# Kernel tuning notes

Hardware: AMD Instinct MI355X
Metric: run time of the kernel (lower is better)

The kernel has to match this reference:

```python
import jax, jax.numpy as jnp
import numpy as np

N_NODES = 50000
N_EDGES = 800000
IN_C = 128
HID_C = 2 * IN_C  # 256
OUT_C = 128
NEG_SLOPE = 0.2


def _gat_layer(x, edge_src, edge_dst, W, a_src, a_dst, b, n_nodes):
    # x: [N, Fin], W: [Fin, Fout], a_src/a_dst: [Fout], b: [Fout]
    h = x @ W                                   # [N, Fout]
    alpha_src = h @ a_src                       # [N]
    alpha_dst = h @ a_dst                       # [N]
    e = alpha_src[edge_src] + alpha_dst[edge_dst]           # [E]
    e = jnp.where(e > 0, e, NEG_SLOPE * e)      # LeakyReLU(0.2)
    # segment softmax over incoming edges of each destination node
    m = jax.ops.segment_max(e, edge_dst, num_segments=n_nodes)  # [N]
    w = jnp.exp(e - m[edge_dst])                               # [E]
    z = jax.ops.segment_sum(w, edge_dst, num_segments=n_nodes)  # [N]
    alpha = w / z[edge_dst]                                     # [E]
    # scatter-aggregate messages
    out = jax.ops.segment_sum(alpha[:, None] * h[edge_src], edge_dst,
                              num_segments=n_nodes)             # [N, Fout]
    return out + b


def setup_inputs() -> dict:
    key = jax.random.key(0)
    ks = jax.random.split(key, 12)
    x = jax.random.normal(ks[0], (N_NODES, IN_C), dtype=jnp.float32)
    edge_index = jax.random.randint(ks[1], (2, N_EDGES), 0, N_NODES, dtype=jnp.int32)
    def glorot(k, shape):
        fan_in = shape[0] if len(shape) == 2 else shape[0]
        return jax.random.normal(k, shape, dtype=jnp.float32) / np.sqrt(fan_in)
    W1 = glorot(ks[2], (IN_C, HID_C))
    a1_src = glorot(ks[3], (HID_C,))
    a1_dst = glorot(ks[4], (HID_C,))
    b1 = jnp.zeros((HID_C,), dtype=jnp.float32)
    W2 = glorot(ks[5], (HID_C, OUT_C))
    a2_src = glorot(ks[6], (OUT_C,))
    a2_dst = glorot(ks[7], (OUT_C,))
    b2 = jnp.zeros((OUT_C,), dtype=jnp.float32)
    return {"x": x, "edge_index": edge_index, "W1": W1, "a1_src": a1_src,
            "a1_dst": a1_dst, "b1": b1, "W2": W2, "a2_src": a2_src,
            "a2_dst": a2_dst, "b2": b2}


def reference(x, edge_index, W1, a1_src, a1_dst, b1, W2, a2_src, a2_dst, b2):
    n = x.shape[0]
    # PyG GATConv default: add self-loops
    loops = jnp.arange(n, dtype=edge_index.dtype)
    src = jnp.concatenate([edge_index[0], loops])
    dst = jnp.concatenate([edge_index[1], loops])
    h = _gat_layer(x, src, dst, W1, a1_src, a1_dst, b1, n)
    h = jax.nn.relu(h)
    out = _gat_layer(h, src, dst, W2, a2_src, a2_dst, b2, n)
    return out
```

## Files before the change

kernel.cpp:

```cpp
#include <hip/hip_runtime.h>
#include <hip/hip_bf16.h>
#include <math.h>

#define N_NODES 50000
#define N_EDGESX 800000
#define E_TOT   (N_EDGESX + N_NODES)
#define IN_C 128
#define HID_C 256
#define OUT_C 128
#define NEG_SLOPE 0.2f

typedef __attribute__((ext_vector_type(8))) short short8;
typedef __attribute__((ext_vector_type(4))) float floatx4;
typedef __attribute__((ext_vector_type(2))) float floatx2;

__device__ __forceinline__ float bf2f(short s) {
    unsigned u = ((unsigned)(unsigned short)s) << 16;
    float f; __builtin_memcpy(&f, &u, 4); return f;
}
__device__ __forceinline__ short f2bf(float f) {
    unsigned u; __builtin_memcpy(&u, &f, 4);
    unsigned r = (u + 0x7FFFu + ((u >> 16) & 1u)) >> 16;
    return (short)r;
}

template<int KROWS, int NCOLS>
__global__ __launch_bounds__(256)
void gemv_p_kernel(const float* __restrict__ W, const float* __restrict__ a_s,
                   const float* __restrict__ a_d, float* __restrict__ ps, float* __restrict__ pd) {
    int t = threadIdx.x;
    int k = t & (KROWS - 1);
    const float* av = (t < KROWS) ? a_s : a_d;
    float* pv = (t < KROWS) ? ps : pd;
    const float* row = W + (size_t)k * NCOLS;
    float s = 0.f;
    for (int n = 0; n < NCOLS; ++n) s += row[n] * av[n];
    pv[k] = s;
}

__global__ __launch_bounds__(256)
void alpha_x_kernel(const float* __restrict__ x, const float* __restrict__ ps,
                    const float* __restrict__ pd, float* __restrict__ as_out,
                    float* __restrict__ ad_out, short* __restrict__ xb) {
    int gt = blockIdx.x * blockDim.x + threadIdx.x;
    int node = gt >> 6, lane = gt & 63;
    if (node >= N_NODES) return;
    floatx2 xv = *(const floatx2*)&x[(size_t)node * IN_C + lane * 2];
    floatx2 s2 = *(const floatx2*)&ps[lane * 2];
    floatx2 d2 = *(const floatx2*)&pd[lane * 2];
    float s = xv[0] * s2[0] + xv[1] * s2[1];
    float d = xv[0] * d2[0] + xv[1] * d2[1];
    unsigned pack = (unsigned)(unsigned short)f2bf(xv[0]) | ((unsigned)(unsigned short)f2bf(xv[1]) << 16);
    *(unsigned*)&xb[(size_t)node * IN_C + lane * 2] = pack;
    #pragma unroll
    for (int off = 32; off; off >>= 1) {
        s += __shfl_down(s, off);
        d += __shfl_down(d, off);
    }
    if (lane == 0) { as_out[node] = s; ad_out[node] = d; }
}

__global__ void count_kernel(const int* __restrict__ dst, int* __restrict__ cnt) {
    int i = blockIdx.x * blockDim.x + threadIdx.x;
    if (i < E_TOT) {
        int d = (i < N_EDGESX) ? dst[i] : (i - N_EDGESX);
        atomicAdd(&cnt[d], 1);
    }
}

#define NBLK ((N_NODES + 1023) / 1024)

__global__ __launch_bounds__(1024)
void scan_a_kernel(const int* __restrict__ cnt, int* __restrict__ row_ptr, int* __restrict__ bsum) {
    __shared__ int buf[1024];
    int tid = threadIdx.x;
    int idx = blockIdx.x * 1024 + tid;
    int v = (idx < N_NODES) ? cnt[idx] : 0;
    buf[tid] = v;
    __syncthreads();
    for (int off = 1; off < 1024; off <<= 1) {
        int t = (tid >= off) ? buf[tid - off] : 0;
        __syncthreads();
        buf[tid] += t;
        __syncthreads();
    }
    if (idx < N_NODES) row_ptr[idx] = buf[tid] - v;
    if (tid == 1023) bsum[blockIdx.x] = buf[1023];
}

__global__ void scan_b_kernel(int* __restrict__ bsum, int* __restrict__ row_ptr) {
    int lane = threadIdx.x;
    int v = (lane < NBLK) ? bsum[lane] : 0;
    int s = v;
    #pragma unroll
    for (int off = 1; off < 64; off <<= 1) {
        int t = __shfl_up(s, off);
        if (lane >= off) s += t;
    }
    if (lane < NBLK) bsum[lane] = s - v;
    if (lane == 63) row_ptr[N_NODES] = s;
}

__global__ __launch_bounds__(1024)
void scan_c_kernel(int* __restrict__ row_ptr, const int* __restrict__ bsum, int* __restrict__ cursor) {
    int idx = blockIdx.x * 1024 + threadIdx.x;
    if (idx < N_NODES) {
        int v = row_ptr[idx] + bsum[blockIdx.x];
        row_ptr[idx] = v;
        cursor[idx] = v;
    }
}

__global__ void scatter_kernel(const int* __restrict__ src, const int* __restrict__ dst,
                               int* __restrict__ cursor, int* __restrict__ esrc) {
    int i = blockIdx.x * blockDim.x + threadIdx.x;
    if (i < E_TOT) {
        int s, d;
        if (i < N_EDGESX) { s = src[i]; d = dst[i]; }
        else { s = i - N_EDGESX; d = s; }
        int pos = atomicAdd(&cursor[d], 1);
        esrc[pos] = s;
    }
}

__global__ __launch_bounds__(256)
void fill_edst_kernel(const int* __restrict__ row_ptr, int* __restrict__ edst) {
    int gt = blockIdx.x * blockDim.x + threadIdx.x;
    int node = gt >> 6, lane = gt & 63;
    if (node >= N_NODES) return;
    int beg = row_ptr[node], end = row_ptr[node + 1];
    for (int i = beg + lane; i < end; i += 64) edst[i] = node;
}

__global__ void ew_kernel(const int* __restrict__ esrc, const int* __restrict__ edst,
                          const float* __restrict__ as_in, const float* __restrict__ ad_in,
                          float* __restrict__ ew) {
    int i = blockIdx.x * blockDim.x + threadIdx.x;
    if (i >= E_TOT) return;
    float e = as_in[esrc[i]] + ad_in[edst[i]];
    ew[i] = e > 0.f ? e : NEG_SLOPE * e;
}

__global__ void splitT_kernel(const float* __restrict__ W, short* __restrict__ th,
                              short* __restrict__ tl, int K, int N) {
    int i = blockIdx.x * blockDim.x + threadIdx.x;
    if (i >= K * N) return;
    int k = i / N, n = i - k * N;
    float f = W[i];
    short hb = f2bf(f);
    th[n * K + k] = hb;
    tl[n * K + k] = f2bf(f - bf2f(hb));
}

template<int K, int OUTMODE>
__global__ __launch_bounds__(256)
void gemm_mfma(const short* __restrict__ Ah, const short* __restrict__ Al,
               const short* __restrict__ Bth, const short* __restrict__ Btl,
               int N, const float* __restrict__ bias,
               short* __restrict__ C0, short* __restrict__ C1) {
    __shared__ short Ah_s[128][40];
    __shared__ short Al_s[128][40];
    __shared__ short Bh_s[64][40];
    __shared__ short Bl_s[64][40];
    int tid = threadIdx.x;
    int lane = tid & 63, wave = tid >> 6;
    int wr = wave >> 1, wc = wave & 1;
    int bm = blockIdx.y * 128, bn = blockIdx.x * 64;
    int l15 = lane & 15, kf = (lane >> 4) * 8;

    floatx4 acc[4][2];
    #pragma unroll
    for (int i = 0; i < 4; ++i)
        #pragma unroll
        for (int j = 0; j < 2; ++j) acc[i][j] = (floatx4){0.f, 0.f, 0.f, 0.f};

    int arow = tid >> 1, ac0 = (tid & 1) * 16;
    int brow = tid >> 2, bc0 = (tid & 3) * 8;
    int agm = bm + arow;
    bool aval = agm < N_NODES;

    for (int k0 = 0; k0 < K; k0 += 32) {
        short8 va0 = {0,0,0,0,0,0,0,0}, va1 = va0, vl0 = va0, vl1 = va0;
        if (aval) {
            const short* pa = Ah + (size_t)agm * K + k0 + ac0;
            va0 = *(const short8*)pa; va1 = *(const short8*)(pa + 8);
            const short* pl = Al + (size_t)agm * K + k0 + ac0;
            vl0 = *(const short8*)pl; vl1 = *(const short8*)(pl + 8);
        }
        *(short8*)&Ah_s[arow][ac0]     = va0;
        *(short8*)&Ah_s[arow][ac0 + 8] = va1;
        *(short8*)&Al_s[arow][ac0]     = vl0;
        *(short8*)&Al_s[arow][ac0 + 8] = vl1;
        {
            const short* pb = Bth + (size_t)(bn + brow) * K + k0 + bc0;
            *(short8*)&Bh_s[brow][bc0] = *(const short8*)pb;
            const short* pb2 = Btl + (size_t)(bn + brow) * K + k0 + bc0;
            *(short8*)&Bl_s[brow][bc0] = *(const short8*)pb2;
        }
        __syncthreads();
        short8 afh[4], afl[4], bfh[2], bfl[2];
        #pragma unroll
        for (int mr = 0; mr < 4; ++mr) {
            int r = wr * 64 + mr * 16 + l15;
            afh[mr] = *(const short8*)&Ah_s[r][kf];
            afl[mr] = *(const short8*)&Al_s[r][kf];
        }
        #pragma unroll
        for (int nr = 0; nr < 2; ++nr) {
            int c = wc * 32 + nr * 16 + l15;
            bfh[nr] = *(const short8*)&Bh_s[c][kf];
            bfl[nr] = *(const short8*)&Bl_s[c][kf];
        }
        #pragma unroll
        for (int mr = 0; mr < 4; ++mr)
            #pragma unroll
            for (int nr = 0; nr < 2; ++nr) {
                acc[mr][nr] = __builtin_amdgcn_mfma_f32_16x16x32_bf16(afh[mr], bfh[nr], acc[mr][nr], 0, 0, 0);
                acc[mr][nr] = __builtin_amdgcn_mfma_f32_16x16x32_bf16(afh[mr], bfl[nr], acc[mr][nr], 0, 0, 0);
                acc[mr][nr] = __builtin_amdgcn_mfma_f32_16x16x32_bf16(afl[mr], bfh[nr], acc[mr][nr], 0, 0, 0);
            }
        __syncthreads();
    }
    float bv[2];
    if (OUTMODE == 2) {
        #pragma unroll
        for (int nr = 0; nr < 2; ++nr) bv[nr] = bias[bn + wc * 32 + nr * 16 + l15];
    }
    #pragma unroll
    for (int mr = 0; mr < 4; ++mr) {
        #pragma unroll
        for (int reg = 0; reg < 4; ++reg) {
            int gr = bm + wr * 64 + mr * 16 + (lane >> 4) * 4 + reg;
            if (gr < N_NODES) {
                #pragma unroll
                for (int nr = 0; nr < 2; ++nr) {
                    int gc = bn + wc * 32 + nr * 16 + l15;
                    float v = acc[mr][nr][reg];
                    if (OUTMODE == 1) {
                        C0[(size_t)gr * N + gc] = f2bf(v);
                    } else {
                        v = fmaxf(v + bv[nr], 0.f);
                        short hb = f2bf(v);
                        C0[(size_t)gr * N + gc] = hb;
                        C1[(size_t)gr * N + gc] = f2bf(v - bf2f(hb));
                    }
                }
            }
        }
    }
}

__global__ __launch_bounds__(256)
void alpha_bf16_128(const short* __restrict__ h, const float* __restrict__ a_src,
                    const float* __restrict__ a_dst, float* __restrict__ as_out,
                    float* __restrict__ ad_out) {
    int gt = blockIdx.x * blockDim.x + threadIdx.x;
    int node = gt >> 6, lane = gt & 63;
    if (node >= N_NODES) return;
    unsigned u = *(const unsigned*)&h[(size_t)node * OUT_C + lane * 2];
    float v0 = bf2f((short)(u & 0xFFFFu));
    float v1 = bf2f((short)(u >> 16));
    floatx2 as2 = *(const floatx2*)&a_src[lane * 2];
    floatx2 ad2 = *(const floatx2*)&a_dst[lane * 2];
    float s = v0 * as2[0] + v1 * as2[1];
    float d = v0 * ad2[0] + v1 * ad2[1];
    #pragma unroll
    for (int off = 32; off; off >>= 1) {
        s += __shfl_down(s, off);
        d += __shfl_down(d, off);
    }
    if (lane == 0) { as_out[node] = s; ad_out[node] = d; }
}

template<int OUT>
__global__ __launch_bounds__(256)
void aggregate_kernel(const short* __restrict__ h, const float* __restrict__ ew,
                      const int* __restrict__ row_ptr, const int* __restrict__ esrc,
                      const float* __restrict__ bias,
                      short* __restrict__ o_hi, short* __restrict__ o_lo,
                      float* __restrict__ o_f32) {
    int gt = blockIdx.x * blockDim.x + threadIdx.x;
    int node = gt >> 6, lane = gt & 63;
    if (node >= N_NODES) return;
    int beg = row_ptr[node], end = row_ptr[node + 1];

    float ml = -1e30f, zl = 0.f;
    for (int i = beg + lane; i < end; i += 64) {
        float e = ew[i];
        float mn = fmaxf(ml, e);
        zl = zl * __expf(ml - mn) + __expf(e - mn);
        ml = mn;
    }
    #pragma unroll
    for (int off = 32; off; off >>= 1) {
        float mo = __shfl_xor(ml, off);
        float zo = __shfl_xor(zl, off);
        float mn = fmaxf(ml, mo);
        zl = zl * __expf(ml - mn) + zo * __expf(mo - mn);
        ml = mn;
    }
    float m = ml;
    float inv_z = 1.f / zl;

    int grp = lane >> 4, l = lane & 15;
    float acc[8] = {};
    int i = beg;
    for (; i + 4 < end; i += 8) {
        int e0 = i + grp;
        int e1 = i + 4 + grp;
        bool v1 = e1 < end;
        int s0 = esrc[e0];
        int s1 = esrc[v1 ? e1 : beg];
        float w0 = __expf(ew[e0] - m) * inv_z;
        float w1 = v1 ? __expf(ew[e1] - m) * inv_z : 0.f;
        short8 hv0 = *(const short8*)&h[(size_t)s0 * 128 + l * 8];
        short8 hv1 = *(const short8*)&h[(size_t)s1 * 128 + l * 8];
        #pragma unroll
        for (int j = 0; j < 8; ++j) acc[j] += w0 * bf2f(hv0[j]);
        #pragma unroll
        for (int j = 0; j < 8; ++j) acc[j] += w1 * bf2f(hv1[j]);
    }
    if (i < end) {
        int e = i + grp;
        bool v = e < end;
        int s = esrc[v ? e : beg];
        float w = v ? __expf(ew[e] - m) * inv_z : 0.f;
        short8 hv = *(const short8*)&h[(size_t)s * 128 + l * 8];
        #pragma unroll
        for (int j = 0; j < 8; ++j) acc[j] += w * bf2f(hv[j]);
    }
    #pragma unroll
    for (int j = 0; j < 8; ++j) {
        acc[j] += __shfl_xor(acc[j], 16);
        acc[j] += __shfl_xor(acc[j], 32);
    }

    if (lane < 16) {
        if (OUT == 0) {
            short8 oh, ol;
            #pragma unroll
            for (int j = 0; j < 8; ++j) {
                short hb = f2bf(acc[j]);
                oh[j] = hb;
                ol[j] = f2bf(acc[j] - bf2f(hb));
            }
            *(short8*)&o_hi[(size_t)node * 128 + l * 8] = oh;
            *(short8*)&o_lo[(size_t)node * 128 + l * 8] = ol;
        } else {
            const float* brow = &bias[l * 8];
            floatx4 o0, o1;
            #pragma unroll
            for (int j = 0; j < 4; ++j) {
                o0[j] = acc[j] + brow[j];
                o1[j] = acc[j + 4] + brow[j + 4];
            }
            float* orow = &o_f32[(size_t)node * 128 + l * 8];
            *(floatx4*)orow = o0;
            *(floatx4*)(orow + 4) = o1;
        }
    }
}

extern "C" void kernel_launch(void* const* d_in, const int* in_sizes, int n_in,
                              void* d_out, int out_size, void* d_ws, size_t ws_size,
                              hipStream_t stream) {
    const float* x   = (const float*)d_in[0];
    const int*   ei  = (const int*)d_in[1];
    const float* W1  = (const float*)d_in[2];
    const float* a1s = (const float*)d_in[3];
    const float* a1d = (const float*)d_in[4];
    const float* b1  = (const float*)d_in[5];
    const float* W2  = (const float*)d_in[6];
    const float* a2s = (const float*)d_in[7];
    const float* a2d = (const float*)d_in[8];
    const float* b2  = (const float*)d_in[9];
    float* out = (float*)d_out;

    const int* e_src = ei;
    const int* e_dst = ei + N_EDGESX;

    char* ws = (char*)d_ws;
    const size_t OFF_XB   = 0;
    const size_t OFF_UH   = 12800000;
    const size_t OFF_UL   = 25600000;
    const size_t OFF_G1H  = 38400000;
    const size_t OFF_G1L  = 64000000;
    const size_t OFF_H2   = 89600000;
    const size_t OFF_W1TH = 102400000;
    const size_t OFF_W1TL = 102465536;
    const size_t OFF_W2TH = 102531072;
    const size_t OFF_W2TL = 102596608;
    const size_t OFF_P1S  = 102662144;
    const size_t OFF_P1D  = 102662656;
    const size_t OFF_AS   = 102663168;
    const size_t OFF_AD   = 102863360;
    const size_t OFF_RP   = 103063552;
    const size_t OFF_CNT  = 103264000;
    const size_t OFF_CUR  = 103464192;
    const size_t OFF_BSUM = 103664384;
    const size_t OFF_ESRC = 103664640;
    const size_t OFF_EDST = 107064640;
    const size_t OFF_EW   = 110464640;

    short* xb   = (short*)(ws + OFF_XB);
    short* uh   = (short*)(ws + OFF_UH);
    short* ul   = (short*)(ws + OFF_UL);
    short* g1h  = (short*)(ws + OFF_G1H);
    short* g1l  = (short*)(ws + OFF_G1L);
    short* h2   = (short*)(ws + OFF_H2);
    short* w1th = (short*)(ws + OFF_W1TH);
    short* w1tl = (short*)(ws + OFF_W1TL);
    short* w2th = (short*)(ws + OFF_W2TH);
    short* w2tl = (short*)(ws + OFF_W2TL);
    float* p1s  = (float*)(ws + OFF_P1S);
    float* p1d  = (float*)(ws + OFF_P1D);
    float* as_b = (float*)(ws + OFF_AS);
    float* ad_b = (float*)(ws + OFF_AD);
    int* row_ptr = (int*)(ws + OFF_RP);
    int* cnt     = (int*)(ws + OFF_CNT);
    int* cursor  = (int*)(ws + OFF_CUR);
    int* bsum    = (int*)(ws + OFF_BSUM);
    int* esrc    = (int*)(ws + OFF_ESRC);
    int* edst    = (int*)(ws + OFF_EDST);
    float* ewb   = (float*)(ws + OFF_EW);

    int egrid = (E_TOT + 255) / 256;
    int ngrid = (N_NODES * 64 + 255) / 256;

    gemv_p_kernel<IN_C, HID_C><<<1, 256, 0, stream>>>(W1, a1s, a1d, p1s, p1d);
    alpha_x_kernel<<<ngrid, 256, 0, stream>>>(x, p1s, p1d, as_b, ad_b, xb);

    hipMemsetAsync(cnt, 0, N_NODES * sizeof(int), stream);
    count_kernel<<<egrid, 256, 0, stream>>>(e_dst, cnt);
    scan_a_kernel<<<NBLK, 1024, 0, stream>>>(cnt, row_ptr, bsum);
    scan_b_kernel<<<1, 64, 0, stream>>>(bsum, row_ptr);
    scan_c_kernel<<<NBLK, 1024, 0, stream>>>(row_ptr, bsum, cursor);
    scatter_kernel<<<egrid, 256, 0, stream>>>(e_src, e_dst, cursor, esrc);
    fill_edst_kernel<<<ngrid, 256, 0, stream>>>(row_ptr, edst);
    ew_kernel<<<egrid, 256, 0, stream>>>(esrc, edst, as_b, ad_b, ewb);

    splitT_kernel<<<(IN_C * HID_C + 255) / 256, 256, 0, stream>>>(W1, w1th, w1tl, IN_C, HID_C);
    splitT_kernel<<<(HID_C * OUT_C + 255) / 256, 256, 0, stream>>>(W2, w2th, w2tl, HID_C, OUT_C);

    aggregate_kernel<0><<<ngrid, 256, 0, stream>>>(xb, ewb, row_ptr, esrc, nullptr, uh, ul, nullptr);
    gemm_mfma<IN_C, 2><<<dim3(HID_C / 64, (N_NODES + 127) / 128), 256, 0, stream>>>(
        uh, ul, w1th, w1tl, HID_C, b1, g1h, g1l);

    gemm_mfma<HID_C, 1><<<dim3(OUT_C / 64, (N_NODES + 127) / 128), 256, 0, stream>>>(
        g1h, g1l, w2th, w2tl, OUT_C, nullptr, h2, nullptr);
    alpha_bf16_128<<<ngrid, 256, 0, stream>>>(h2, a2s, a2d, as_b, ad_b);
    ew_kernel<<<egrid, 256, 0, stream>>>(esrc, edst, as_b, ad_b, ewb);
    aggregate_kernel<1><<<ngrid, 256, 0, stream>>>(h2, ewb, row_ptr, esrc, b2, nullptr, nullptr, out);
}
```

Before: 365.2 us.

## Build CSR via two-pass bucketed binning with shared-memory atomics, fuse edge weights

Replaces the global-atomic count and scatter CSR build with a two-level bucketing scheme. Edges are first binned into 100-node buckets using per-block shared histograms and a staging buffer. Per-bucket kernels then count and scatter with shared-memory atomics. The first-layer edge-weight computation is fused into the bucket scatter. Each bucket's staging capacity is fixed, so edges beyond that cap would be silently dropped on skewed graphs.

```diff
diff --git a/kernel.cpp b/kernel.cpp
--- a/kernel.cpp
+++ b/kernel.cpp
@@ -9,6 +9,12 @@
 #define HID_C 256
 #define OUT_C 128
 #define NEG_SLOPE 0.2f
+
+#define NPB   100
+#define NBUCK ((N_NODES + NPB - 1) / NPB)
+#define BCAP  2560
+#define EPB   4096
+#define NABLK ((E_TOT + EPB - 1) / EPB)
 
 typedef __attribute__((ext_vector_type(8))) short short8;
 typedef __attribute__((ext_vector_type(4))) float floatx4;
@@ -60,11 +66,77 @@
     if (lane == 0) { as_out[node] = s; ad_out[node] = d; }
 }
 
-__global__ void count_kernel(const int* __restrict__ dst, int* __restrict__ cnt) {
-    int i = blockIdx.x * blockDim.x + threadIdx.x;
-    if (i < E_TOT) {
+__global__ __launch_bounds__(256)
+void binA_kernel(const int* __restrict__ src, const int* __restrict__ dst,
+                 int* __restrict__ bcnt, int2* __restrict__ stage) {
+    __shared__ int hist[NBUCK];
+    __shared__ int base[NBUCK];
+    for (int b = threadIdx.x; b < NBUCK; b += 256) hist[b] = 0;
+    __syncthreads();
+    int e0 = blockIdx.x * EPB;
+    int e1 = min(e0 + EPB, E_TOT);
+    for (int i = e0 + threadIdx.x; i < e1; i += 256) {
         int d = (i < N_EDGESX) ? dst[i] : (i - N_EDGESX);
-        atomicAdd(&cnt[d], 1);
+        atomicAdd(&hist[d / NPB], 1);
+    }
+    __syncthreads();
+    for (int b = threadIdx.x; b < NBUCK; b += 256) {
+        int c = hist[b];
+        base[b] = c ? atomicAdd(&bcnt[b], c) : 0;
+        hist[b] = 0;
+    }
+    __syncthreads();
+    for (int i = e0 + threadIdx.x; i < e1; i += 256) {
+        int s, d;
+        if (i < N_EDGESX) { s = src[i]; d = dst[i]; }
+        else { s = i - N_EDGESX; d = s; }
+        int b = d / NPB;
+        int off = base[b] + atomicAdd(&hist[b], 1);
+        if (off < BCAP) stage[(size_t)b * BCAP + off] = make_int2(s, d);
+    }
+}
+
+__global__ __launch_bounds__(128)
+void bucket_count_kernel(const int* __restrict__ bcnt, const int2* __restrict__ stage,
+                         int* __restrict__ cnt) {
+    __shared__ int lc[NPB];
+    int b = blockIdx.x;
+    for (int t = threadIdx.x; t < NPB; t += 128) lc[t] = 0;
+    __syncthreads();
+    int n = min(bcnt[b], BCAP);
+    const int2* sp = stage + (size_t)b * BCAP;
+    for (int i = threadIdx.x; i < n; i += 128)
+        atomicAdd(&lc[sp[i].y - b * NPB], 1);
+    __syncthreads();
+    int nb = b * NPB;
+    for (int t = threadIdx.x; t < NPB; t += 128)
+        if (nb + t < N_NODES) cnt[nb + t] = lc[t];
+}
+
+__global__ __launch_bounds__(128)
+void bucket_scatter_kernel(const int* __restrict__ bcnt, const int2* __restrict__ stage,
+                           const int* __restrict__ row_ptr, const float* __restrict__ as_in,
+                           const float* __restrict__ ad_in, int* __restrict__ esrc,
+                           float* __restrict__ ew) {
+    __shared__ int cur[NPB];
+    __shared__ float adl[NPB];
+    int b = blockIdx.x;
+    int nb = b * NPB;
+    for (int t = threadIdx.x; t < NPB; t += 128) {
+        int node = nb + t;
+        cur[t] = (node < N_NODES) ? row_ptr[node] : 0;
+        adl[t] = (node < N_NODES) ? ad_in[node] : 0.f;
+    }
+    __syncthreads();
+    int n = min(bcnt[b], BCAP);
+    const int2* sp = stage + (size_t)b * BCAP;
+    for (int i = threadIdx.x; i < n; i += 128) {
+        int2 e = sp[i];
+        int li = e.y - nb;
+        int pos = atomicAdd(&cur[li], 1);
+        esrc[pos] = e.x;
+        float v = as_in[e.x] + adl[li];
+        ew[pos] = v > 0.f ? v : NEG_SLOPE * v;
     }
 }
 
@@ -102,25 +174,9 @@
 }
 
 __global__ __launch_bounds__(1024)
-void scan_c_kernel(int* __restrict__ row_ptr, const int* __restrict__ bsum, int* __restrict__ cursor) {
+void scan_c_kernel(int* __restrict__ row_ptr, const int* __restrict__ bsum) {
     int idx = blockIdx.x * 1024 + threadIdx.x;
-    if (idx < N_NODES) {
-        int v = row_ptr[idx] + bsum[blockIdx.x];
-        row_ptr[idx] = v;
-        cursor[idx] = v;
-    }
-}
-
-__global__ void scatter_kernel(const int* __restrict__ src, const int* __restrict__ dst,
-                               int* __restrict__ cursor, int* __restrict__ esrc) {
-    int i = blockIdx.x * blockDim.x + threadIdx.x;
-    if (i < E_TOT) {
-        int s, d;
-        if (i < N_EDGESX) { s = src[i]; d = dst[i]; }
-        else { s = i - N_EDGESX; d = s; }
-        int pos = atomicAdd(&cursor[d], 1);
-        esrc[pos] = s;
-    }
+    if (idx < N_NODES) row_ptr[idx] += bsum[blockIdx.x];
 }
 
 __global__ __launch_bounds__(256)
@@ -380,27 +436,28 @@
     const int* e_dst = ei + N_EDGESX;
 
     char* ws = (char*)d_ws;
-    const size_t OFF_XB   = 0;
-    const size_t OFF_UH   = 12800000;
-    const size_t OFF_UL   = 25600000;
-    const size_t OFF_G1H  = 38400000;
-    const size_t OFF_G1L  = 64000000;
-    const size_t OFF_H2   = 89600000;
-    const size_t OFF_W1TH = 102400000;
-    const size_t OFF_W1TL = 102465536;
-    const size_t OFF_W2TH = 102531072;
-    const size_t OFF_W2TL = 102596608;
-    const size_t OFF_P1S  = 102662144;
-    const size_t OFF_P1D  = 102662656;
-    const size_t OFF_AS   = 102663168;
-    const size_t OFF_AD   = 102863360;
-    const size_t OFF_RP   = 103063552;
-    const size_t OFF_CNT  = 103264000;
-    const size_t OFF_CUR  = 103464192;
-    const size_t OFF_BSUM = 103664384;
-    const size_t OFF_ESRC = 103664640;
-    const size_t OFF_EDST = 107064640;
-    const size_t OFF_EW   = 110464640;
+    const size_t OFF_XB    = 0;
+    const size_t OFF_UH    = 12800000;
+    const size_t OFF_UL    = 25600000;
+    const size_t OFF_G1H   = 38400000;
+    const size_t OFF_G1L   = 64000000;
+    const size_t OFF_H2    = 89600000;
+    const size_t OFF_W1TH  = 102400000;
+    const size_t OFF_W1TL  = 102465536;
+    const size_t OFF_W2TH  = 102531072;
+    const size_t OFF_W2TL  = 102596608;
+    const size_t OFF_P1S   = 102662144;
+    const size_t OFF_P1D   = 102662656;
+    const size_t OFF_AS    = 102663168;
+    const size_t OFF_AD    = 102863360;
+    const size_t OFF_RP    = 103063552;
+    const size_t OFF_CNT   = 103264000;
+    const size_t OFF_BSUM  = 103464192;
+    const size_t OFF_BCNT  = 103464448;
+    const size_t OFF_ESRC  = 103466496;
+    const size_t OFF_EDST  = 106866496;
+    const size_t OFF_EW    = 110266496;
+    const size_t OFF_STAGE = 113666496;
 
     short* xb   = (short*)(ws + OFF_XB);
     short* uh   = (short*)(ws + OFF_UH);
@@ -418,11 +475,12 @@
     float* ad_b = (float*)(ws + OFF_AD);
     int* row_ptr = (int*)(ws + OFF_RP);
     int* cnt     = (int*)(ws + OFF_CNT);
-    int* cursor  = (int*)(ws + OFF_CUR);
     int* bsum    = (int*)(ws + OFF_BSUM);
+    int* bcnt    = (int*)(ws + OFF_BCNT);
     int* esrc    = (int*)(ws + OFF_ESRC);
     int* edst    = (int*)(ws + OFF_EDST);
     float* ewb   = (float*)(ws + OFF_EW);
+    int2* stage  = (int2*)(ws + OFF_STAGE);
 
     int egrid = (E_TOT + 255) / 256;
     int ngrid = (N_NODES * 64 + 255) / 256;
@@ -430,14 +488,14 @@
     gemv_p_kernel<IN_C, HID_C><<<1, 256, 0, stream>>>(W1, a1s, a1d, p1s, p1d);
     alpha_x_kernel<<<ngrid, 256, 0, stream>>>(x, p1s, p1d, as_b, ad_b, xb);
 
-    hipMemsetAsync(cnt, 0, N_NODES * sizeof(int), stream);
-    count_kernel<<<egrid, 256, 0, stream>>>(e_dst, cnt);
+    hipMemsetAsync(bcnt, 0, NBUCK * sizeof(int), stream);
+    binA_kernel<<<NABLK, 256, 0, stream>>>(e_src, e_dst, bcnt, stage);
+    bucket_count_kernel<<<NBUCK, 128, 0, stream>>>(bcnt, stage, cnt);
     scan_a_kernel<<<NBLK, 1024, 0, stream>>>(cnt, row_ptr, bsum);
     scan_b_kernel<<<1, 64, 0, stream>>>(bsum, row_ptr);
-    scan_c_kernel<<<NBLK, 1024, 0, stream>>>(row_ptr, bsum, cursor);
-    scatter_kernel<<<egrid, 256, 0, stream>>>(e_src, e_dst, cursor, esrc);
+    scan_c_kernel<<<NBLK, 1024, 0, stream>>>(row_ptr, bsum);
+    bucket_scatter_kernel<<<NBUCK, 128, 0, stream>>>(bcnt, stage, row_ptr, as_b, ad_b, esrc, ewb);
     fill_edst_kernel<<<ngrid, 256, 0, stream>>>(row_ptr, edst);
-    ew_kernel<<<egrid, 256, 0, stream>>>(esrc, edst, as_b, ad_b, ewb);
 
     splitT_kernel<<<(IN_C * HID_C + 255) / 256, 256, 0, stream>>>(W1, w1th, w1tl, IN_C, HID_C);
     splitT_kernel<<<(HID_C * OUT_C + 255) / 256, 256, 0, stream>>>(W2, w2th, w2tl, HID_C, OUT_C);
```

After: 309.2 us. -15.3%, faster.
